# Kernel tuning notes

Measured on AMD Instinct MI355X. Metric: run time of the kernel, lower is better.

## Reference

```python
import jax, jax.numpy as jnp
import numpy as np

N, E = 100000, 1600000
N_IN, NHID, HEADS, NOUT = 64, 16, 4, 64
NEG_SLOPE = 0.2


def _p(key, shape, scale=0.1):
    return jax.random.normal(key, shape, dtype=jnp.float32) * scale


def setup_inputs() -> dict:
    key = jax.random.key(0)
    ks = jax.random.split(key, 16)
    H, C1 = HEADS, NHID
    inp = {
        "x": jax.random.normal(ks[0], (N, N_IN), dtype=jnp.float32),
        "edge_index": jax.random.randint(ks[1], (2, E), 0, N, dtype=jnp.int64),
        "frame_mask": jnp.ones((N,), dtype=bool),
        # layer 1: GATv2Conv(N_IN -> NHID, heads=H, concat=True)
        "Wl1": _p(ks[2], (N_IN, H * C1)),
        "bl1": jnp.zeros((H * C1,), jnp.float32),
        "Wr1": _p(ks[3], (N_IN, H * C1)),
        "br1": jnp.zeros((H * C1,), jnp.float32),
        "att1": _p(ks[4], (H, C1)),
        "bo1": jnp.zeros((H * C1,), jnp.float32),
        # layer 2: GATv2Conv(H*NHID -> NOUT, heads=H, concat=False)
        "Wl2": _p(ks[5], (H * C1, H * NOUT)),
        "bl2": jnp.zeros((H * NOUT,), jnp.float32),
        "Wr2": _p(ks[6], (H * C1, H * NOUT)),
        "br2": jnp.zeros((H * NOUT,), jnp.float32),
        "att2": _p(ks[7], (H, NOUT)),
        "bo2": jnp.zeros((NOUT,), jnp.float32),
    }
    return inp


def gatv2_layer(x, src, dst, Wl, bl, Wr, br, att, bo, concat):
    n = x.shape[0]
    H, C = att.shape
    xl = (x @ Wl + bl).reshape(n, H, C)  # source-side transform
    xr = (x @ Wr + br).reshape(n, H, C)  # target-side transform
    # per-edge GATv2 attention: att . leaky_relu(xl[j] + xr[i])
    e = jax.nn.leaky_relu(xl[src] + xr[dst], NEG_SLOPE)  # [E', H, C]
    score = jnp.einsum('ehc,hc->eh', e, att)             # [E', H]
    # scatter-softmax over edges grouped by destination node
    m = jax.ops.segment_max(score, dst, num_segments=n)
    ex = jnp.exp(score - m[dst])
    denom = jax.ops.segment_sum(ex, dst, num_segments=n)
    alpha = ex / (denom[dst] + 1e-16)                    # [E', H]
    out = jax.ops.segment_sum(alpha[:, :, None] * xl[src], dst, num_segments=n)
    out = out.reshape(n, H * C) if concat else out.mean(axis=1)
    return out + bo


def reference(x, edge_index, frame_mask, Wl1, bl1, Wr1, br1, att1, bo1,
              Wl2, bl2, Wr2, br2, att2, bo2):
    n = x.shape[0]
    loops = jnp.arange(n, dtype=edge_index.dtype)
    src = jnp.concatenate([edge_index[0], loops])  # add self-loops (PyG default)
    dst = jnp.concatenate([edge_index[1], loops])
    h = gatv2_layer(x, src, dst, Wl1, bl1, Wr1, br1, att1, bo1, concat=True)
    h = jax.nn.relu(h)
    h = gatv2_layer(h, src, dst, Wl2, bl2, Wr2, br2, att2, bo2, concat=False)
    return jax.nn.relu(h)
```

## Files before the change

kernel.cpp:

```cpp
#include <hip/hip_runtime.h>
#include <hip/hip_bf16.h>
#include <cstdint>
#include <cstddef>

#define NNODES 100000
#define NEDGES 1600000
#define EPLUS  (NEDGES + NNODES)
#define NHEADS 4
#define NB     ((NNODES + 255) / 256)

typedef __hip_bfloat16 bf16;
typedef unsigned short u16;
typedef __attribute__((ext_vector_type(8))) short bf16x8;
typedef __attribute__((ext_vector_type(4))) float f32x4;

#define F_X    0
#define F_WL1  1
#define F_BL1  2
#define F_WR1  3
#define F_BR1  4
#define F_ATT1 5
#define F_BO1  6
#define F_WL2  7
#define F_BL2  8
#define F_WR2  9
#define F_BR2  10
#define F_ATT2 11
#define F_BO2  12
#define F_EI64 13

__device__ __forceinline__ float u2f(u16 s) { return __uint_as_float(((unsigned)s) << 16); }
__device__ __forceinline__ u16  f2u(float f) {
    return __bfloat16_as_ushort(__float2bfloat16(f));
}
__device__ __forceinline__ float ld_any(const void* p, long i, int f32) {
    return f32 ? ((const float*)p)[i] : u2f(((const u16*)p)[i]);
}

__global__ void detect_all(const u16* x, const u16* Wl1, const u16* bl1,
                           const u16* Wr1, const u16* br1, const u16* att1,
                           const u16* bo1, const u16* Wl2, const u16* bl2,
                           const u16* Wr2, const u16* br2, const u16* att2,
                           const u16* bo2, const int* ei, int* flags) {
    const int t = threadIdx.x;
    const u16* ptrs[13] = {x, Wl1, bl1, Wr1, br1, att1, bo1,
                           Wl2, bl2, Wr2, br2, att2, bo2};
    const int cnts[13] = {NNODES * 64, 64 * 64, 64, 64 * 64, 64, 64, 64,
                          64 * 256, 256, 64 * 256, 256, 256, 64};
    if (t < 13) {
        const u16* p = ptrs[t];
        const int cnt = cnts[t];
        int weird = 0, n = 0;
        for (int k = 0; k < 128; ++k) {
            int idx = 2 * k;
            if (idx >= cnt) break;
            u16 v = p[idx];
            n++;
            int ex = (v >> 7) & 0xFF;
            if (v != 0 && (ex < 96 || ex > 143)) weird++;
        }
        flags[t] = (weird * 4 > n) ? 1 : 0;
    } else if (t == 13) {
        int any = 0;
        for (int k = 0; k < 64; ++k) any |= ei[2 * k + 1];
        flags[F_EI64] = (any == 0) ? 1 : 0;
    }
}

__device__ __forceinline__ void edge_sd(const int* __restrict__ ei, int i64,
                                        int e, int& s, int& d) {
    if (e >= NEDGES) { s = d = e - NEDGES; return; }
    if (i64) {
        const long long* p = (const long long*)ei;
        s = (int)p[e]; d = (int)p[NEDGES + e];
    } else {
        s = ei[e]; d = ei[NEDGES + e];
    }
    s = min(max(s, 0), NNODES - 1);
    d = min(max(d, 0), NNODES - 1);
}

__global__ __launch_bounds__(256)
void conv_x(const void* __restrict__ x, const int* __restrict__ flags,
            u16* __restrict__ xc) {
    const long i4 = ((long)blockIdx.x * 256 + threadIdx.x) * 4;
    if (i4 >= (long)NNODES * 64) return;
    if (flags[F_X]) {
        const float4 v = *(const float4*)((const float*)x + i4);
        ushort4 o; o.x = f2u(v.x); o.y = f2u(v.y); o.z = f2u(v.z); o.w = f2u(v.w);
        *(ushort4*)(xc + i4) = o;
    } else {
        *(ushort4*)(xc + i4) = *(const ushort4*)((const u16*)x + i4);
    }
}

template<int M>
__global__ __launch_bounds__(256)
void conv_w(const void* __restrict__ W, const int* __restrict__ flags, int fwi,
            u16* __restrict__ wt) {
    const int idx = blockIdx.x * 256 + threadIdx.x;
    if (idx >= M * 64) return;
    const int m = idx >> 6, k = idx & 63;
    wt[idx] = f2u(ld_any(W, (long)k * M + m, flags[fwi]));
}

__global__ void conv_b(const void* bl1, const void* br1, const void* bl2,
                       const void* br2, const int* __restrict__ flags,
                       u16* __restrict__ out) {
    const int t = threadIdx.x;
    if (t < 64)       out[t] = f2u(ld_any(bl1, t,       flags[F_BL1]));
    else if (t < 128) out[t] = f2u(ld_any(br1, t - 64,  flags[F_BR1]));
    else if (t < 384) out[t] = f2u(ld_any(bl2, t - 128, flags[F_BL2]));
    else if (t < 640) out[t] = f2u(ld_any(br2, t - 384, flags[F_BR2]));
}

__global__ __launch_bounds__(256)
void hist_kernel(const int* __restrict__ ei, const int* __restrict__ flags,
                 int* __restrict__ cnt) {
    const int e = blockIdx.x * 256 + threadIdx.x;
    if (e >= NEDGES) return;
    int d;
    if (flags[F_EI64]) d = (int)((const long long*)ei)[NEDGES + e];
    else               d = ei[NEDGES + e];
    d = min(max(d, 0), NNODES - 1);
    atomicAdd(&cnt[d], 1);
}

__global__ __launch_bounds__(256)
void scan1_kernel(const int* __restrict__ cnt, int* __restrict__ tmp,
                  int* __restrict__ bsum) {
    __shared__ int sh[256];
    const int idx = blockIdx.x * 256 + threadIdx.x;
    int v = (idx < NNODES) ? cnt[idx] + 1 : 0;
    sh[threadIdx.x] = v;
    __syncthreads();
    for (int off = 1; off < 256; off <<= 1) {
        int t = (threadIdx.x >= off) ? sh[threadIdx.x - off] : 0;
        __syncthreads();
        sh[threadIdx.x] += t;
        __syncthreads();
    }
    if (idx < NNODES) tmp[idx] = sh[threadIdx.x];
    if (threadIdx.x == 255) bsum[blockIdx.x] = sh[255];
}

__global__ __launch_bounds__(512)
void scan2_kernel(int* __restrict__ bsum) {
    __shared__ int sh[512];
    const int t = threadIdx.x;
    sh[t] = (t < NB) ? bsum[t] : 0;
    __syncthreads();
    for (int off = 1; off < 512; off <<= 1) {
        int v = (t >= off) ? sh[t - off] : 0;
        __syncthreads();
        sh[t] += v;
        __syncthreads();
    }
    if (t < NB) bsum[t] = sh[t];
}

__global__ __launch_bounds__(256)
void scan3_kernel(const int* __restrict__ tmp, const int* __restrict__ bsum,
                  int* __restrict__ row_ptr) {
    const int idx = blockIdx.x * 256 + threadIdx.x;
    if (idx < NNODES) {
        int off = (blockIdx.x > 0) ? bsum[blockIdx.x - 1] : 0;
        row_ptr[idx + 1] = tmp[idx] + off;
    }
    if (idx == 0) row_ptr[0] = 0;
}

__global__ __launch_bounds__(256)
void fill_kernel(const int* __restrict__ ei, const int* __restrict__ flags,
                 const int* __restrict__ row_ptr, int* __restrict__ cur,
                 int* __restrict__ csr_src) {
    const int e = blockIdx.x * 256 + threadIdx.x;
    if (e >= EPLUS) return;
    int s, d;
    edge_sd(ei, flags[F_EI64], e, s, d);
    int slot = row_ptr[d] + atomicAdd(&cur[d], 1);
    csr_src[slot] = s;
}

template<int M, int RPB>
__global__ __launch_bounds__(256)
void gemm_mfma(const u16* __restrict__ xc, const u16* __restrict__ wt,
               const u16* __restrict__ bc, u16* __restrict__ out) {
    constexpr int MT = RPB / 16;
    constexpr int NT = M / 64;
    const int wave = threadIdx.x >> 6;
    const int lane = threadIdx.x & 63;
    const int quad = lane >> 4;
    const int l16  = lane & 15;
    const int row0 = blockIdx.x * RPB;
    const int col0 = wave * (M / 4);

    bf16x8 bfrag[NT][2];
#pragma unroll
    for (int nt = 0; nt < NT; ++nt)
#pragma unroll
        for (int c = 0; c < 2; ++c)
            bfrag[nt][c] = *(const bf16x8*)(wt +
                ((size_t)(col0 + nt * 16 + l16) * 64 + c * 32 + quad * 8));

    f32x4 acc[MT][NT];
#pragma unroll
    for (int mt = 0; mt < MT; ++mt)
#pragma unroll
        for (int nt = 0; nt < NT; ++nt)
            acc[mt][nt] = f32x4{0.f, 0.f, 0.f, 0.f};

#pragma unroll
    for (int mt = 0; mt < MT; ++mt) {
        int row = row0 + mt * 16 + l16;
        row = (row < NNODES) ? row : (NNODES - 1);
#pragma unroll
        for (int c = 0; c < 2; ++c) {
            bf16x8 afrag = *(const bf16x8*)(xc + ((size_t)row * 64 + c * 32 + quad * 8));
#pragma unroll
            for (int nt = 0; nt < NT; ++nt)
                acc[mt][nt] = __builtin_amdgcn_mfma_f32_16x16x32_bf16(
                    afrag, bfrag[nt][c], acc[mt][nt], 0, 0, 0);
        }
    }

#pragma unroll
    for (int mt = 0; mt < MT; ++mt) {
#pragma unroll
        for (int nt = 0; nt < NT; ++nt) {
            const int col = col0 + nt * 16 + l16;
            const float bias = u2f(bc[col]);
#pragma unroll
            for (int r = 0; r < 4; ++r) {
                const int row = row0 + mt * 16 + quad * 4 + r;
                if (row < NNODES)
                    out[(size_t)row * M + col] = f2u(acc[mt][nt][r] + bias);
            }
        }
    }
}

template<int HC, bool MEAN, typename TO>
__global__ __launch_bounds__(256)
void fused_gat(const u16* __restrict__ xl, const u16* __restrict__ xr,
               const int* __restrict__ row_ptr, const int* __restrict__ csr_src,
               const void* __restrict__ att, const void* __restrict__ bo,
               const int* __restrict__ flags, int fai, int fbi,
               TO* __restrict__ out) {
    constexpr int VEC = HC / 64;
    const int d = blockIdx.x * 4 + (threadIdx.x >> 6);
    if (d >= NNODES) return;
    const int lane = threadIdx.x & 63;
    const int fatt = flags[fai];

    float attv[VEC], rv[VEC];
#pragma unroll
    for (int j = 0; j < VEC; ++j)
        attv[j] = ld_any(att, lane * VEC + j, fatt);
    if constexpr (VEC == 4) {
        ushort4 r = *(const ushort4*)(xr + (size_t)d * HC + lane * 4);
        rv[0]=u2f(r.x); rv[1]=u2f(r.y); rv[2]=u2f(r.z); rv[3]=u2f(r.w);
    } else {
        rv[0] = u2f(xr[(size_t)d * HC + lane]);
    }

    const int beg = row_ptr[d], end = row_ptr[d + 1];
    float denom = 1e-16f;
    float acc[VEC];
#pragma unroll
    for (int j = 0; j < VEC; ++j) acc[j] = 0.f;

    int s_cur = csr_src[beg];
    ushort4 a4; u16 a1;
    if constexpr (VEC == 4)
        a4 = *(const ushort4*)(xl + (size_t)s_cur * HC + lane * 4);
    else
        a1 = xl[(size_t)s_cur * HC + lane];

    for (int i = beg; i < end; ++i) {
        float lv[VEC];
        if constexpr (VEC == 4) {
            lv[0]=u2f(a4.x); lv[1]=u2f(a4.y); lv[2]=u2f(a4.z); lv[3]=u2f(a4.w);
        } else {
            lv[0] = u2f(a1);
        }
        if (i + 1 < end) {
            int s_nxt = csr_src[i + 1];
            if constexpr (VEC == 4)
                a4 = *(const ushort4*)(xl + (size_t)s_nxt * HC + lane * 4);
            else
                a1 = xl[(size_t)s_nxt * HC + lane];
        }
        float part = 0.f;
#pragma unroll
        for (int j = 0; j < VEC; ++j) {
            float v = lv[j] + rv[j];
            v = (v > 0.f) ? v : 0.2f * v;
            part = fmaf(v, attv[j], part);
        }
#pragma unroll
        for (int off = 8; off >= 1; off >>= 1)
            part += __shfl_xor(part, off, 64);
        float ex = __expf(fminf(fmaxf(part, -60.f), 60.f));
        denom += ex;
#pragma unroll
        for (int j = 0; j < VEC; ++j)
            acc[j] = fmaf(ex, lv[j], acc[j]);
    }

    const float inv = 1.f / denom;
    if constexpr (MEAN) {
#pragma unroll
        for (int j = 0; j < VEC; ++j) {
            acc[j] *= inv;
            acc[j] += __shfl_xor(acc[j], 16, 64);
            acc[j] += __shfl_xor(acc[j], 32, 64);
        }
        if (lane < 16) {
            const int fbo = flags[fbi];
            float4 o;
            float* op = (float*)&o;
#pragma unroll
            for (int j = 0; j < VEC; ++j) {
                float v = acc[j] * 0.25f + ld_any(bo, lane * 4 + j, fbo);
                op[j] = (v > 0.f) ? v : 0.f;
            }
            *(float4*)((float*)out + (size_t)d * 64 + lane * 4) = o;
        }
    } else {
        const int fbo = flags[fbi];
        float v = acc[0] * inv + ld_any(bo, lane, fbo);
        v = (v > 0.f) ? v : 0.f;
        ((u16*)out)[(size_t)d * 64 + lane] = f2u(v);
    }
}

__global__ void plant_kernel(float* out, float code) {
    if (code > 0.f) out[0] = code;
}

extern "C" void kernel_launch(void* const* d_in, const int* in_sizes, int n_in,
                              void* d_out, int out_size, void* d_ws, size_t ws_size,
                              hipStream_t stream) {
    int ix = -1, iei = -1;
    int i4096[2], i16384[2], i64s[5], i256[3];
    int c4 = 0, c16 = 0, c64 = 0, c256 = 0;
    bool extra = false;
    for (int i = 0; i < n_in; ++i) {
        int sz = in_sizes[i];
        if (sz == 6400000)      { if (ix < 0) ix = i; else extra = true; }
        else if (sz == 3200000) { if (iei < 0) iei = i; else extra = true; }
        else if (sz == 4096)    { if (c4  < 2) i4096[c4]  = i; c4++;  }
        else if (sz == 16384)   { if (c16 < 2) i16384[c16] = i; c16++; }
        else if (sz == 64)      { if (c64 < 5) i64s[c64]  = i; c64++; }
        else if (sz == 256)     { if (c256 < 3) i256[c256] = i; c256++; }
        else if (sz == 100000 || sz == 1) {  }
        else extra = true;
    }
    bool ok = (ix >= 0) && (iei >= 0) && (c4 == 2) && (c16 == 2)
              && (c64 == 5) && (c256 == 3) && !extra;
    float code = 0.f;
    if (!ok) {
        code = 50000.f + 100.f * (float)n_in;
        ix = 0; iei = 1;
        i4096[0] = 3;  i4096[1] = 5;
        i64s[0] = 4; i64s[1] = 6; i64s[2] = 7; i64s[3] = 8; i64s[4] = 14;
        i16384[0] = 9; i16384[1] = 11;
        i256[0] = 10; i256[1] = 12; i256[2] = 13;
    }

    const u16* x    = (const u16*)d_in[ix];
    const int* ei   = (const int*)d_in[iei];
    const u16* Wl1  = (const u16*)d_in[i4096[0]];
    const u16* Wr1  = (const u16*)d_in[i4096[1]];
    const u16* bl1  = (const u16*)d_in[i64s[0]];
    const u16* br1  = (const u16*)d_in[i64s[1]];
    const u16* att1 = (const u16*)d_in[i64s[2]];
    const u16* bo1  = (const u16*)d_in[i64s[3]];
    const u16* bo2  = (const u16*)d_in[i64s[4]];
    const u16* Wl2  = (const u16*)d_in[i16384[0]];
    const u16* Wr2  = (const u16*)d_in[i16384[1]];
    const u16* bl2  = (const u16*)d_in[i256[0]];
    const u16* br2  = (const u16*)d_in[i256[1]];
    const u16* att2 = (const u16*)d_in[i256[2]];

    char* ws = (char*)d_ws;
    u16* xlb     = (u16*)(ws);
    u16* xrb     = (u16*)(ws + 51200000);
    u16* hbuf    = (u16*)(ws + 102400000);
    u16* xc      = (u16*)(ws + 115200000);
    int* row_ptr = (int*)(ws + 128000000);
    int* cnt     = (int*)(ws + 128400016);
    int* tmp     = (int*)(ws + 128800016);
    int* bsum    = (int*)(ws + 129201600 - 1584);
    int* csr_src = (int*)(ws + 129201600);
    u16* wt1l    = (u16*)(ws + 136001600);
    u16* wt1r    = (u16*)(ws + 136009792);
    u16* wt2l    = (u16*)(ws + 136017984);
    u16* wt2r    = (u16*)(ws + 136050752);
    u16* bcs     = (u16*)(ws + 136083520);
    int* flags   = (int*)(ws + 136084800);
    const size_t need = 136084864;
    if (ws_size < need) {
        float c2 = 60000.f + (float)(ws_size >> 20);
        code = (c2 > code) ? c2 : code;
    }

    const int node_grid = (NNODES + 3) / 4;
    const int e_grid    = (NEDGES + 255) / 256;
    const int ep_grid   = (EPLUS + 255) / 256;

    detect_all<<<1, 64, 0, stream>>>(x, Wl1, bl1, Wr1, br1, att1, bo1,
                                     Wl2, bl2, Wr2, br2, att2, bo2, ei, flags);

    conv_x<<<(NNODES * 64 / 4 + 255) / 256, 256, 0, stream>>>(x, flags, xc);
    conv_w<64><<<16, 256, 0, stream>>>(Wl1, flags, F_WL1, wt1l);
    conv_w<64><<<16, 256, 0, stream>>>(Wr1, flags, F_WR1, wt1r);
    conv_w<256><<<64, 256, 0, stream>>>(Wl2, flags, F_WL2, wt2l);
    conv_w<256><<<64, 256, 0, stream>>>(Wr2, flags, F_WR2, wt2r);
    conv_b<<<1, 640, 0, stream>>>(bl1, br1, bl2, br2, flags, bcs);

    (void)hipMemsetAsync(cnt, 0, (size_t)NNODES * 4, stream);
    hist_kernel<<<e_grid, 256, 0, stream>>>(ei, flags, cnt);
    scan1_kernel<<<NB, 256, 0, stream>>>(cnt, tmp, bsum);
    scan2_kernel<<<1, 512, 0, stream>>>(bsum);
    scan3_kernel<<<NB, 256, 0, stream>>>(tmp, bsum, row_ptr);
    (void)hipMemsetAsync(cnt, 0, (size_t)NNODES * 4, stream);
    fill_kernel<<<ep_grid, 256, 0, stream>>>(ei, flags, row_ptr, cnt, csr_src);

    gemm_mfma<64, 128><<<(NNODES + 127) / 128, 256, 0, stream>>>(xc, wt1l, bcs,       xlb);
    gemm_mfma<64, 128><<<(NNODES + 127) / 128, 256, 0, stream>>>(xc, wt1r, bcs + 64,  xrb);
    fused_gat<64, false, u16><<<node_grid, 256, 0, stream>>>(
        xlb, xrb, row_ptr, csr_src, att1, bo1, flags, F_ATT1, F_BO1, hbuf);

    gemm_mfma<256, 64><<<(NNODES + 63) / 64, 256, 0, stream>>>(hbuf, wt2l, bcs + 128, xlb);
    gemm_mfma<256, 64><<<(NNODES + 63) / 64, 256, 0, stream>>>(hbuf, wt2r, bcs + 384, xrb);
    fused_gat<256, true, float><<<node_grid, 256, 0, stream>>>(
        xlb, xrb, row_ptr, csr_src, att2, bo2, flags, F_ATT2, F_BO2, (float*)d_out);

    plant_kernel<<<1, 1, 0, stream>>>((float*)d_out, code);
}
```

Baseline: 731.8 us.

## Process four edges per wavefront in fused GAT and merge conversion kernels

The fused GATv2 aggregation kernel now splits each 64-lane wavefront into four groups of 16 lanes, each handling a different incoming edge, with wider per-lane vectors. It reduces partial sums across groups at the end. This is meant to raise memory-level parallelism on the gather and shorten the per-edge shuffle reduction. The max-subtraction clamp on the scores is dropped. Separately, the x/weight/bias conversion kernels and the degree histogram are merged into one launch to cut launch overhead.

```diff
diff --git a/kernel.cpp b/kernel.cpp
--- a/kernel.cpp
+++ b/kernel.cpp
@@ -35,6 +35,10 @@
 }
 __device__ __forceinline__ float ld_any(const void* p, long i, int f32) {
     return f32 ? ((const float*)p)[i] : u2f(((const u16*)p)[i]);
+}
+__device__ __forceinline__ void cvt_pair(unsigned p, float& lo, float& hi) {
+    lo = __uint_as_float(p << 16);
+    hi = __uint_as_float(p & 0xffff0000u);
 }
 
 __global__ void detect_all(const u16* x, const u16* Wl1, const u16* bl1,
@@ -80,50 +84,65 @@
     d = min(max(d, 0), NNODES - 1);
 }
 
-__global__ __launch_bounds__(256)
-void conv_x(const void* __restrict__ x, const int* __restrict__ flags,
-            u16* __restrict__ xc) {
-    const long i4 = ((long)blockIdx.x * 256 + threadIdx.x) * 4;
-    if (i4 >= (long)NNODES * 64) return;
-    if (flags[F_X]) {
-        const float4 v = *(const float4*)((const float*)x + i4);
-        ushort4 o; o.x = f2u(v.x); o.y = f2u(v.y); o.z = f2u(v.z); o.w = f2u(v.w);
-        *(ushort4*)(xc + i4) = o;
-    } else {
-        *(ushort4*)(xc + i4) = *(const ushort4*)((const u16*)x + i4);
-    }
-}
-
-template<int M>
-__global__ __launch_bounds__(256)
-void conv_w(const void* __restrict__ W, const int* __restrict__ flags, int fwi,
-            u16* __restrict__ wt) {
-    const int idx = blockIdx.x * 256 + threadIdx.x;
-    if (idx >= M * 64) return;
-    const int m = idx >> 6, k = idx & 63;
-    wt[idx] = f2u(ld_any(W, (long)k * M + m, flags[fwi]));
-}
-
-__global__ void conv_b(const void* bl1, const void* br1, const void* bl2,
-                       const void* br2, const int* __restrict__ flags,
-                       u16* __restrict__ out) {
-    const int t = threadIdx.x;
-    if (t < 64)       out[t] = f2u(ld_any(bl1, t,       flags[F_BL1]));
-    else if (t < 128) out[t] = f2u(ld_any(br1, t - 64,  flags[F_BR1]));
-    else if (t < 384) out[t] = f2u(ld_any(bl2, t - 128, flags[F_BL2]));
-    else if (t < 640) out[t] = f2u(ld_any(br2, t - 384, flags[F_BR2]));
-}
-
-__global__ __launch_bounds__(256)
-void hist_kernel(const int* __restrict__ ei, const int* __restrict__ flags,
-                 int* __restrict__ cnt) {
-    const int e = blockIdx.x * 256 + threadIdx.x;
-    if (e >= NEDGES) return;
-    int d;
-    if (flags[F_EI64]) d = (int)((const long long*)ei)[NEDGES + e];
-    else               d = ei[NEDGES + e];
-    d = min(max(d, 0), NNODES - 1);
-    atomicAdd(&cnt[d], 1);
+#define XB 6250
+#define WB 160
+#define BB 3
+#define HB 6250
+__global__ __launch_bounds__(256)
+void conv_all(const void* __restrict__ x,
+              const void* __restrict__ Wl1, const void* __restrict__ Wr1,
+              const void* __restrict__ Wl2, const void* __restrict__ Wr2,
+              const void* __restrict__ bl1, const void* __restrict__ br1,
+              const void* __restrict__ bl2, const void* __restrict__ br2,
+              const int* __restrict__ ei, const int* __restrict__ flags,
+              u16* __restrict__ xc, u16* __restrict__ wt1l, u16* __restrict__ wt1r,
+              u16* __restrict__ wt2l, u16* __restrict__ wt2r,
+              u16* __restrict__ bcs, int* __restrict__ cnt) {
+    int b = blockIdx.x;
+    if (b < XB) {
+        const long i4 = ((long)b * 256 + threadIdx.x) * 4;
+        if (i4 < (long)NNODES * 64) {
+            if (flags[F_X]) {
+                const float4 v = *(const float4*)((const float*)x + i4);
+                ushort4 o; o.x=f2u(v.x); o.y=f2u(v.y); o.z=f2u(v.z); o.w=f2u(v.w);
+                *(ushort4*)(xc + i4) = o;
+            } else {
+                *(ushort4*)(xc + i4) = *(const ushort4*)((const u16*)x + i4);
+            }
+        }
+        return;
+    }
+    b -= XB;
+    if (b < WB) {
+        const int e = b * 256 + threadIdx.x;
+        const void* W; u16* wt; int M, fwi, local;
+        if (e < 4096)        { W = Wl1; wt = wt1l; M = 64;  fwi = F_WL1; local = e; }
+        else if (e < 8192)   { W = Wr1; wt = wt1r; M = 64;  fwi = F_WR1; local = e - 4096; }
+        else if (e < 24576)  { W = Wl2; wt = wt2l; M = 256; fwi = F_WL2; local = e - 8192; }
+        else                 { W = Wr2; wt = wt2r; M = 256; fwi = F_WR2; local = e - 24576; }
+        const int m = local >> 6, k = local & 63;
+        wt[local] = f2u(ld_any(W, (long)k * M + m, flags[fwi]));
+        return;
+    }
+    b -= WB;
+    if (b < BB) {
+        const int t = b * 256 + threadIdx.x;
+        if (t < 64)       bcs[t] = f2u(ld_any(bl1, t,       flags[F_BL1]));
+        else if (t < 128) bcs[t] = f2u(ld_any(br1, t - 64,  flags[F_BR1]));
+        else if (t < 384) bcs[t] = f2u(ld_any(bl2, t - 128, flags[F_BL2]));
+        else if (t < 640) bcs[t] = f2u(ld_any(br2, t - 384, flags[F_BR2]));
+        return;
+    }
+    b -= BB;
+    {
+        const int e = b * 256 + threadIdx.x;
+        if (e >= NEDGES) return;
+        int d;
+        if (flags[F_EI64]) d = (int)((const long long*)ei)[NEDGES + e];
+        else               d = ei[NEDGES + e];
+        d = min(max(d, 0), NNODES - 1);
+        atomicAdd(&cnt[d], 1);
+    }
 }
 
 __global__ __launch_bounds__(256)
@@ -247,21 +266,26 @@
                const void* __restrict__ att, const void* __restrict__ bo,
                const int* __restrict__ flags, int fai, int fbi,
                TO* __restrict__ out) {
-    constexpr int VEC = HC / 64;
+    constexpr int VEC = HC / 16;
+    constexpr int NU  = VEC / 2;
     const int d = blockIdx.x * 4 + (threadIdx.x >> 6);
     if (d >= NNODES) return;
     const int lane = threadIdx.x & 63;
+    const int q = lane >> 4;
+    const int l = lane & 15;
     const int fatt = flags[fai];
 
     float attv[VEC], rv[VEC];
 #pragma unroll
     for (int j = 0; j < VEC; ++j)
-        attv[j] = ld_any(att, lane * VEC + j, fatt);
-    if constexpr (VEC == 4) {
-        ushort4 r = *(const ushort4*)(xr + (size_t)d * HC + lane * 4);
-        rv[0]=u2f(r.x); rv[1]=u2f(r.y); rv[2]=u2f(r.z); rv[3]=u2f(r.w);
-    } else {
-        rv[0] = u2f(xr[(size_t)d * HC + lane]);
+        attv[j] = ld_any(att, l * VEC + j, fatt);
+    {
+        const unsigned* rp = (const unsigned*)(xr + (size_t)d * HC + l * VEC);
+#pragma unroll
+        for (int u = 0; u < NU; ++u) {
+            unsigned p = rp[u];
+            cvt_pair(p, rv[2 * u], rv[2 * u + 1]);
+        }
     }
 
     const int beg = row_ptr[d], end = row_ptr[d + 1];
@@ -270,68 +294,87 @@
 #pragma unroll
     for (int j = 0; j < VEC; ++j) acc[j] = 0.f;
 
-    int s_cur = csr_src[beg];
-    ushort4 a4; u16 a1;
-    if constexpr (VEC == 4)
-        a4 = *(const ushort4*)(xl + (size_t)s_cur * HC + lane * 4);
-    else
-        a1 = xl[(size_t)s_cur * HC + lane];
-
-    for (int i = beg; i < end; ++i) {
+    unsigned raw[NU];
+    {
+        int e0 = beg + q;
+        int idx = (e0 < end) ? e0 : (end - 1);
+        const unsigned* lp = (const unsigned*)(xl + (size_t)csr_src[idx] * HC + l * VEC);
+#pragma unroll
+        for (int u = 0; u < NU; ++u) raw[u] = lp[u];
+    }
+
+    for (int base = beg; base < end; base += 4) {
         float lv[VEC];
-        if constexpr (VEC == 4) {
-            lv[0]=u2f(a4.x); lv[1]=u2f(a4.y); lv[2]=u2f(a4.z); lv[3]=u2f(a4.w);
-        } else {
-            lv[0] = u2f(a1);
-        }
-        if (i + 1 < end) {
-            int s_nxt = csr_src[i + 1];
-            if constexpr (VEC == 4)
-                a4 = *(const ushort4*)(xl + (size_t)s_nxt * HC + lane * 4);
-            else
-                a1 = xl[(size_t)s_nxt * HC + lane];
+#pragma unroll
+        for (int u = 0; u < NU; ++u) cvt_pair(raw[u], lv[2 * u], lv[2 * u + 1]);
+        if (base + 4 < end) {
+            int en = base + 4 + q;
+            int idx = (en < end) ? en : (end - 1);
+            const unsigned* lp = (const unsigned*)(xl + (size_t)csr_src[idx] * HC + l * VEC);
+#pragma unroll
+            for (int u = 0; u < NU; ++u) raw[u] = lp[u];
         }
         float part = 0.f;
 #pragma unroll
         for (int j = 0; j < VEC; ++j) {
             float v = lv[j] + rv[j];
-            v = (v > 0.f) ? v : 0.2f * v;
+            v = fmaxf(v, 0.2f * v);
             part = fmaf(v, attv[j], part);
         }
-#pragma unroll
-        for (int off = 8; off >= 1; off >>= 1)
-            part += __shfl_xor(part, off, 64);
-        float ex = __expf(fminf(fmaxf(part, -60.f), 60.f));
+        part += __shfl_xor(part, 1, 64);
+        part += __shfl_xor(part, 2, 64);
+        float ex = __expf(fminf(part, 60.f));
+        ex = (base + q < end) ? ex : 0.f;
         denom += ex;
 #pragma unroll
         for (int j = 0; j < VEC; ++j)
             acc[j] = fmaf(ex, lv[j], acc[j]);
     }
 
+    denom += __shfl_xor(denom, 16, 64);
+    denom += __shfl_xor(denom, 32, 64);
+#pragma unroll
+    for (int j = 0; j < VEC; ++j) {
+        acc[j] += __shfl_xor(acc[j], 16, 64);
+        acc[j] += __shfl_xor(acc[j], 32, 64);
+    }
     const float inv = 1.f / denom;
+
     if constexpr (MEAN) {
 #pragma unroll
         for (int j = 0; j < VEC; ++j) {
             acc[j] *= inv;
-            acc[j] += __shfl_xor(acc[j], 16, 64);
-            acc[j] += __shfl_xor(acc[j], 32, 64);
-        }
+            acc[j] += __shfl_xor(acc[j], 4, 64);
+            acc[j] += __shfl_xor(acc[j], 8, 64);
+        }
+        if (lane < 4) {
+            const int fbo = flags[fbi];
+            float* po = (float*)out + (size_t)d * 64 + l * 16;
+#pragma unroll
+            for (int g = 0; g < 4; ++g) {
+                float4 o;
+                float* op = (float*)&o;
+#pragma unroll
+                for (int k = 0; k < 4; ++k) {
+                    int c = l * 16 + g * 4 + k;
+                    float v = acc[g * 4 + k] * 0.25f + ld_any(bo, c, fbo);
+                    op[k] = (v > 0.f) ? v : 0.f;
+                }
+                *(float4*)(po + g * 4) = o;
+            }
+        }
+    } else {
         if (lane < 16) {
             const int fbo = flags[fbi];
-            float4 o;
-            float* op = (float*)&o;
+            ushort4 o;
+            u16* op = (u16*)&o;
 #pragma unroll
             for (int j = 0; j < VEC; ++j) {
-                float v = acc[j] * 0.25f + ld_any(bo, lane * 4 + j, fbo);
-                op[j] = (v > 0.f) ? v : 0.f;
+                float v = acc[j] * inv + ld_any(bo, l * 4 + j, fbo);
+                op[j] = f2u((v > 0.f) ? v : 0.f);
             }
-            *(float4*)((float*)out + (size_t)d * 64 + lane * 4) = o;
-        }
-    } else {
-        const int fbo = flags[fbi];
-        float v = acc[0] * inv + ld_any(bo, lane, fbo);
-        v = (v > 0.f) ? v : 0.f;
-        ((u16*)out)[(size_t)d * 64 + lane] = f2u(v);
+            *(ushort4*)((u16*)out + (size_t)d * 64 + l * 4) = o;
+        }
     }
 }
 
@@ -392,7 +435,7 @@
     int* row_ptr = (int*)(ws + 128000000);
     int* cnt     = (int*)(ws + 128400016);
     int* tmp     = (int*)(ws + 128800016);
-    int* bsum    = (int*)(ws + 129201600 - 1584);
+    int* bsum    = (int*)(ws + 129200016);
     int* csr_src = (int*)(ws + 129201600);
     u16* wt1l    = (u16*)(ws + 136001600);
     u16* wt1r    = (u16*)(ws + 136009792);
@@ -407,21 +450,16 @@
     }
 
     const int node_grid = (NNODES + 3) / 4;
-    const int e_grid    = (NEDGES + 255) / 256;
     const int ep_grid   = (EPLUS + 255) / 256;
 
     detect_all<<<1, 64, 0, stream>>>(x, Wl1, bl1, Wr1, br1, att1, bo1,
                                      Wl2, bl2, Wr2, br2, att2, bo2, ei, flags);
 
-    conv_x<<<(NNODES * 64 / 4 + 255) / 256, 256, 0, stream>>>(x, flags, xc);
-    conv_w<64><<<16, 256, 0, stream>>>(Wl1, flags, F_WL1, wt1l);
-    conv_w<64><<<16, 256, 0, stream>>>(Wr1, flags, F_WR1, wt1r);
-    conv_w<256><<<64, 256, 0, stream>>>(Wl2, flags, F_WL2, wt2l);
-    conv_w<256><<<64, 256, 0, stream>>>(Wr2, flags, F_WR2, wt2r);
-    conv_b<<<1, 640, 0, stream>>>(bl1, br1, bl2, br2, flags, bcs);
-
     (void)hipMemsetAsync(cnt, 0, (size_t)NNODES * 4, stream);
-    hist_kernel<<<e_grid, 256, 0, stream>>>(ei, flags, cnt);
+    conv_all<<<XB + WB + BB + HB, 256, 0, stream>>>(
+        x, Wl1, Wr1, Wl2, Wr2, bl1, br1, bl2, br2, ei, flags,
+        xc, wt1l, wt1r, wt2l, wt2r, bcs, cnt);
+
     scan1_kernel<<<NB, 256, 0, stream>>>(cnt, tmp, bsum);
     scan2_kernel<<<1, 512, 0, stream>>>(bsum);
     scan3_kernel<<<NB, 256, 0, stream>>>(tmp, bsum, row_ptr);
```

New measurement: 782.0 us. 6.9% more time.
